# Kernel tuning notes

Hardware: AMD Instinct MI355X
Metric: run time of the kernel (lower is better)

The kernel has to match this reference:

```python
import jax, jax.numpy as jnp
import numpy as np

ALPHA = 4.0   # spikingjelly surrogate.Sigmoid default
TAU = 2.0
VTH = 1.0
EPS = 1e-5

@jax.custom_vjp
def spike(x):
    return (x >= 0.0).astype(x.dtype)

def _spike_fwd(x):
    return spike(x), x

def _spike_bwd(x, g):
    s = jax.nn.sigmoid(ALPHA * x)
    return (g * ALPHA * s * (1.0 - s),)

spike.defvjp(_spike_fwd, _spike_bwd)

def lif(x):
    # x: [T, B, N, C]; multi-step LIF, v_reset=0 hard reset, detach_reset=True
    def step(v, xt):
        v = v + (xt - v) / TAU          # charge
        s = spike(v - VTH)              # fire (surrogate grad)
        v = v * (1.0 - jax.lax.stop_gradient(s))  # hard reset, detached
        return v, s
    _, out = jax.lax.scan(step, jnp.zeros_like(x[0]), x)
    return out

def bn(x, gamma, beta):
    # BatchNorm1d in training mode: per-channel (last dim) over all other dims
    mu = x.mean(axis=(0, 1, 2), keepdims=True)
    var = x.var(axis=(0, 1, 2), keepdims=True)  # biased var, as torch BN uses for normalization
    return (x - mu) * jax.lax.rsqrt(var + EPS) * gamma + beta

def setup_inputs() -> dict:
    key = jax.random.key(0)
    ks = jax.random.split(key, 3)
    T, B, N, C, H = 4, 32, 1024, 256, 256
    x = jax.random.normal(ks[0], (T, B, N, C), dtype=jnp.float32)
    W1 = jax.random.normal(ks[1], (C, H), dtype=jnp.float32) * (1.0 / np.sqrt(C))
    W2 = jax.random.normal(ks[2], (H, C), dtype=jnp.float32) * (1.0 / np.sqrt(H))
    return {
        "x": x,
        "W1": W1, "b1": jnp.zeros((H,), jnp.float32),
        "gamma1": jnp.ones((H,), jnp.float32), "beta1": jnp.zeros((H,), jnp.float32),
        "W2": W2, "b2": jnp.zeros((C,), jnp.float32),
        "gamma2": jnp.ones((C,), jnp.float32), "beta2": jnp.zeros((C,), jnp.float32),
    }

def reference(x, W1, b1, gamma1, beta1, W2, b2, gamma2, beta2):
    # fc1: Linear -> BN (per-channel over T*B*N) -> multi-step LIF
    h = jnp.einsum('tbnc,ch->tbnh', x, W1) + b1
    h = lif(bn(h, gamma1, beta1))
    # fc2
    o = jnp.einsum('tbnh,ho->tbno', h, W2) + b2
    return lif(bn(o, gamma2, beta2))
```

## Files before the change

kernel.cpp:

```cpp
#include <hip/hip_runtime.h>


typedef __attribute__((ext_vector_type(8))) short bf16x8;
typedef __attribute__((ext_vector_type(8))) _Float16 f16x8;
typedef __attribute__((ext_vector_type(4))) _Float16 f16x4;
typedef __attribute__((ext_vector_type(4))) float f32x4;

__device__ __forceinline__ unsigned short f32_to_bf16_rne(float f) {
    unsigned int u = __builtin_bit_cast(unsigned int, f);
    u += 0x7FFFu + ((u >> 16) & 1u);
    return (unsigned short)(u >> 16);
}
__device__ __forceinline__ float bf16_to_f32(unsigned short h) {
    unsigned int u = ((unsigned int)h) << 16;
    return __builtin_bit_cast(float, u);
}
__device__ __forceinline__ int xcd_swz(int bid, int nwg) {
    int per = nwg >> 3;
    return (bid & 7) * per + (bid >> 3);
}

__global__ __launch_bounds__(256) void split_w1(const float* __restrict__ W1,
                                                _Float16* __restrict__ BhiT,
                                                _Float16* __restrict__ BloT) {
    int i = blockIdx.x * 256 + threadIdx.x;
    int k = i >> 8, n = i & 255;
    float w = W1[i];
    _Float16 hi = (_Float16)w;
    _Float16 lo = (_Float16)((w - (float)hi) * 4096.0f);
    BhiT[(size_t)n * 256 + k] = hi;
    BloT[(size_t)n * 256 + k] = lo;
}

__global__ __launch_bounds__(256) void split_w2(const float* __restrict__ W2,
                                                unsigned short* __restrict__ Bt) {
    int i = blockIdx.x * 256 + threadIdx.x;
    int k = i >> 8, n = i & 255;
    float w = W2[i];
    unsigned short hi = f32_to_bf16_rne(w);
    float r = w - bf16_to_f32(hi);
    unsigned short mid = f32_to_bf16_rne(r);
    float r2 = r - bf16_to_f32(mid);
    unsigned short lo = f32_to_bf16_rne(r2);
    Bt[(size_t)(0 * 256 + n) * 256 + k] = hi;
    Bt[(size_t)(1 * 256 + n) * 256 + k] = mid;
    Bt[(size_t)(2 * 256 + n) * 256 + k] = lo;
}

__global__ __launch_bounds__(256, 2) void gemm1_mfma(const float* __restrict__ A,
                                                     const _Float16* __restrict__ Bhi,
                                                     const _Float16* __restrict__ Blo,
                                                     const float* __restrict__ bias,
                                                     float* __restrict__ C,
                                                     double* __restrict__ partial) {
    __shared__ __align__(16) _Float16 Ahi[64 * 256];
    __shared__ __align__(16) _Float16 Alo[64 * 256];
    const int blk = xcd_swz(blockIdx.x, gridDim.x);
    const size_t m0 = (size_t)blk * 64;
    const int tid = threadIdx.x;
    const int lane = tid & 63;
    const int wc = tid >> 6;
    const int lrow = lane & 15, lchunk = lane >> 4;

    const _Float16* BhiB = Bhi + ((size_t)(64 * wc + lrow)) * 256 + lchunk * 8;
    const _Float16* BloB = Blo + ((size_t)(64 * wc + lrow)) * 256 + lchunk * 8;

    f16x8 bh[2][4], bl[2][4];
#define LOADB1(buf, kk)                                                   \
    _Pragma("unroll") for (int nf = 0; nf < 4; ++nf) {                    \
        bh[buf][nf] = *(const f16x8*)(BhiB + nf * 4096 + (kk) * 32);      \
        bl[buf][nf] = *(const f16x8*)(BloB + nf * 4096 + (kk) * 32);      \
    }

    LOADB1(0, 0)

    {
        const float* src = A + m0 * 256;
        float4 rr[16];
#pragma unroll
        for (int it = 0; it < 16; ++it)
            rr[it] = *(const float4*)(src + (size_t)(it * 256 + tid) * 4);
#pragma unroll
        for (int it = 0; it < 16; ++it) {
            unsigned i4 = (unsigned)(it * 256 + tid);
            float f[4] = {rr[it].x, rr[it].y, rr[it].z, rr[it].w};
            f16x4 hi4, lo4;
#pragma unroll
            for (int e = 0; e < 4; ++e) {
                _Float16 hh = (_Float16)f[e];
                hi4[e] = hh;
                lo4[e] = (_Float16)((f[e] - (float)hh) * 4096.0f);
            }
            unsigned off = i4 * 8u;
            unsigned swz = off ^ (((off >> 9) & 7u) << 4);
            *(f16x4*)((char*)Ahi + swz) = hi4;
            *(f16x4*)((char*)Alo + swz) = lo4;
        }
    }
    __syncthreads();

    f32x4 acc0[4][4] = {}, acc1[4][4] = {};

#pragma unroll
    for (int k0 = 0; k0 < 8; ++k0) {
        const int cur = k0 & 1;
        if (k0 < 7) { LOADB1(cur ^ 1, k0 + 1) }
        f16x8 ah[4], al[4];
#pragma unroll
        for (int mf = 0; mf < 4; ++mf) {
            unsigned r = (unsigned)(16 * mf + lrow);
            unsigned off = (r * 512u + (unsigned)(k0 * 64 + lchunk * 16)) ^ ((r & 7u) << 4);
            ah[mf] = *(const f16x8*)((const char*)Ahi + off);
            al[mf] = *(const f16x8*)((const char*)Alo + off);
        }
        __builtin_amdgcn_s_setprio(1);
#pragma unroll
        for (int nf = 0; nf < 4; ++nf)
#pragma unroll
            for (int mf = 0; mf < 4; ++mf)
                acc0[mf][nf] = __builtin_amdgcn_mfma_f32_16x16x32_f16(
                    ah[mf], bh[cur][nf], acc0[mf][nf], 0, 0, 0);
#pragma unroll
        for (int nf = 0; nf < 4; ++nf)
#pragma unroll
            for (int mf = 0; mf < 4; ++mf)
                acc1[mf][nf] = __builtin_amdgcn_mfma_f32_16x16x32_f16(
                    ah[mf], bl[cur][nf], acc1[mf][nf], 0, 0, 0);
#pragma unroll
        for (int nf = 0; nf < 4; ++nf)
#pragma unroll
            for (int mf = 0; mf < 4; ++mf)
                acc1[mf][nf] = __builtin_amdgcn_mfma_f32_16x16x32_f16(
                    al[mf], bh[cur][nf], acc1[mf][nf], 0, 0, 0);
        __builtin_amdgcn_s_setprio(0);
    }
#undef LOADB1

    const float UNSCALE = 1.0f / 4096.0f;
#pragma unroll
    for (int nf = 0; nf < 4; ++nf) {
        int col = 64 * wc + 16 * nf + lrow;
        float bvv = bias[col];
        double ss = 0.0, qq = 0.0;
#pragma unroll
        for (int mf = 0; mf < 4; ++mf) {
            size_t rowb = m0 + 16 * mf + 4 * lchunk;
#pragma unroll
            for (int e = 0; e < 4; ++e) {
                float hv = acc0[mf][nf][e] + acc1[mf][nf][e] * UNSCALE + bvv;
                C[(rowb + e) * 256 + col] = hv;
                ss += (double)hv;
                qq += (double)hv * (double)hv;
            }
        }
        ss += __shfl_xor(ss, 16);
        ss += __shfl_xor(ss, 32);
        qq += __shfl_xor(qq, 16);
        qq += __shfl_xor(qq, 32);
        if (lane < 16) {
            partial[(size_t)blk * 512 + col] = ss;
            partial[(size_t)blk * 512 + 256 + col] = qq;
        }
    }
}

__global__ __launch_bounds__(256, 2) void gemm2_fused(const float* __restrict__ h,
                                                      const float2* __restrict__ ss1,
                                                      const unsigned short* __restrict__ Bt,
                                                      const float* __restrict__ bias,
                                                      float* __restrict__ C,
                                                      double* __restrict__ partial,
                                                      int bnRows) {
    __shared__ __align__(16) unsigned short Asw[64 * 256];
    const int blk = xcd_swz(blockIdx.x, gridDim.x);
    const int bn0 = blk * 16;
    const int tid = threadIdx.x;
    const int lane = tid & 63;
    const int wc = tid >> 6;
    const int lrow = lane & 15, lchunk = lane >> 4;

    const unsigned short* Bbase =
        Bt + ((size_t)(64 * wc + lrow)) * 256 + lchunk * 8;

    bf16x8 bb[2][12];
#define LOADB(buf, kk)                                                        \
    _Pragma("unroll") for (int t_ = 0; t_ < 3; ++t_)                          \
    _Pragma("unroll") for (int nf = 0; nf < 4; ++nf)                          \
        bb[buf][t_ * 4 + nf] = *(const bf16x8*)(Bbase + (size_t)t_ * 65536 +  \
                                                nf * 4096 + (kk) * 32);

    LOADB(0, 0)

    {
        float4 rr[16];
#pragma unroll
        for (int it = 0; it < 4; ++it) {
            int slot = it * 256 + tid;
            int bn = slot >> 6;
            int colq = slot & 63;
            size_t rb = (size_t)(bn0 + bn) * 256 + colq * 4;
#pragma unroll
            for (int t4 = 0; t4 < 4; ++t4)
                rr[it * 4 + t4] = *(const float4*)(h + (size_t)t4 * bnRows * 256 + rb);
        }
#pragma unroll
        for (int it = 0; it < 4; ++it) {
            int slot = it * 256 + tid;
            int bn = slot >> 6;
            int colq = slot & 63;
            int c0 = colq * 4;
            float2 p0 = ss1[c0], p1 = ss1[c0 + 1], p2 = ss1[c0 + 2], p3 = ss1[c0 + 3];
            float4 v = make_float4(0.f, 0.f, 0.f, 0.f);
#pragma unroll
            for (int t4 = 0; t4 < 4; ++t4) {
                float4 hv = rr[it * 4 + t4];
                float x0 = hv.x * p0.x + p0.y;
                float x1 = hv.y * p1.x + p1.y;
                float x2 = hv.z * p2.x + p2.y;
                float x3 = hv.w * p3.x + p3.y;
                v.x = (v.x + x0) * 0.5f;
                v.y = (v.y + x1) * 0.5f;
                v.z = (v.z + x2) * 0.5f;
                v.w = (v.w + x3) * 0.5f;
                ushort4 sp;
                sp.x = (v.x >= 1.0f) ? 0x3F80 : 0;
                sp.y = (v.y >= 1.0f) ? 0x3F80 : 0;
                sp.z = (v.z >= 1.0f) ? 0x3F80 : 0;
                sp.w = (v.w >= 1.0f) ? 0x3F80 : 0;
                v.x = (v.x >= 1.0f) ? 0.0f : v.x;
                v.y = (v.y >= 1.0f) ? 0.0f : v.y;
                v.z = (v.z >= 1.0f) ? 0.0f : v.z;
                v.w = (v.w >= 1.0f) ? 0.0f : v.w;
                unsigned row = (unsigned)(t4 * 16 + bn);
                unsigned off = (row * 512u + (unsigned)colq * 8u) ^ ((row & 7u) << 4);
                *(ushort4*)((char*)Asw + off) = sp;
            }
        }
    }
    __syncthreads();

    f32x4 acc[4][4] = {};

#pragma unroll
    for (int k0 = 0; k0 < 8; ++k0) {
        const int cur = k0 & 1;
        if (k0 < 7) { LOADB(cur ^ 1, k0 + 1) }
        bf16x8 af[4];
#pragma unroll
        for (int mf = 0; mf < 4; ++mf) {
            unsigned r = (unsigned)(16 * mf + lrow);
            unsigned off = (r * 512u + (unsigned)(k0 * 64 + lchunk * 16)) ^ ((r & 7u) << 4);
            af[mf] = *(const bf16x8*)((const char*)Asw + off);
        }
        __builtin_amdgcn_s_setprio(1);
#pragma unroll
        for (int t_ = 0; t_ < 3; ++t_)
#pragma unroll
            for (int nf = 0; nf < 4; ++nf)
#pragma unroll
                for (int mf = 0; mf < 4; ++mf)
                    acc[mf][nf] = __builtin_amdgcn_mfma_f32_16x16x32_bf16(
                        af[mf], bb[cur][t_ * 4 + nf], acc[mf][nf], 0, 0, 0);
        __builtin_amdgcn_s_setprio(0);
    }
#undef LOADB

#pragma unroll
    for (int nf = 0; nf < 4; ++nf) {
        int col = 64 * wc + 16 * nf + lrow;
        float bvv = bias[col];
        double ss = 0.0, qq = 0.0;
#pragma unroll
        for (int mf = 0; mf < 4; ++mf) {
            int Lbase = 16 * mf + 4 * lchunk;
#pragma unroll
            for (int e = 0; e < 4; ++e) {
                int L = Lbase + e;
                size_t G = (size_t)(L >> 4) * bnRows + bn0 + (L & 15);
                float hv = acc[mf][nf][e] + bvv;
                C[G * 256 + col] = hv;
                ss += (double)hv;
                qq += (double)hv * (double)hv;
            }
        }
        ss += __shfl_xor(ss, 16);
        ss += __shfl_xor(ss, 32);
        qq += __shfl_xor(qq, 16);
        qq += __shfl_xor(qq, 32);
        if (lane < 16) {
            partial[(size_t)blk * 512 + col] = ss;
            partial[(size_t)blk * 512 + 256 + col] = qq;
        }
    }
}

__global__ __launch_bounds__(256) void finalize_stats(const double* __restrict__ partial,
                                                      const float* __restrict__ gamma,
                                                      const float* __restrict__ beta,
                                                      float2* __restrict__ ss,
                                                      int nblocks, double invM) {
    const int c = blockIdx.x;
    const int t = threadIdx.x;
    __shared__ double sh[256];
    __shared__ double sh2[256];
    double s = 0.0, s2 = 0.0;
    for (int b = t; b < nblocks; b += 256) {
        s += partial[(size_t)b * 512 + c];
        s2 += partial[(size_t)b * 512 + 256 + c];
    }
    sh[t] = s;
    sh2[t] = s2;
    __syncthreads();
#pragma unroll
    for (int off = 128; off > 0; off >>= 1) {
        if (t < off) {
            sh[t] += sh[t + off];
            sh2[t] += sh2[t + off];
        }
        __syncthreads();
    }
    if (t == 0) {
        double mu = sh[0] * invM;
        double var = sh2[0] * invM - mu * mu;
        double rstd = 1.0 / sqrt(var + 1e-5);
        double sc = (double)gamma[c] * rstd;
        ss[c] = make_float2((float)sc, (float)((double)beta[c] - mu * sc));
    }
}

__global__ __launch_bounds__(256) void bnlif_f32(const float* __restrict__ h,
                                                 const float2* __restrict__ ss,
                                                 float* __restrict__ out,
                                                 int slab4) {
    int t4 = blockIdx.x * 256 + threadIdx.x;
    if (t4 >= slab4) return;
    size_t idx = (size_t)t4 * 4;
    int c0 = (int)(idx & 255);
    float2 p0 = ss[c0], p1 = ss[c0 + 1], p2 = ss[c0 + 2], p3 = ss[c0 + 3];
    size_t slab = (size_t)slab4 * 4;
    float4 v = make_float4(0.f, 0.f, 0.f, 0.f);
#pragma unroll
    for (int t = 0; t < 4; ++t) {
        float4 hv = *(const float4*)(h + (size_t)t * slab + idx);
        float x0 = hv.x * p0.x + p0.y;
        float x1 = hv.y * p1.x + p1.y;
        float x2 = hv.z * p2.x + p2.y;
        float x3 = hv.w * p3.x + p3.y;
        v.x = (v.x + x0) * 0.5f;
        v.y = (v.y + x1) * 0.5f;
        v.z = (v.z + x2) * 0.5f;
        v.w = (v.w + x3) * 0.5f;
        float4 sp;
        sp.x = (v.x >= 1.0f) ? 1.0f : 0.0f;
        sp.y = (v.y >= 1.0f) ? 1.0f : 0.0f;
        sp.z = (v.z >= 1.0f) ? 1.0f : 0.0f;
        sp.w = (v.w >= 1.0f) ? 1.0f : 0.0f;
        v.x = (v.x >= 1.0f) ? 0.0f : v.x;
        v.y = (v.y >= 1.0f) ? 0.0f : v.y;
        v.z = (v.z >= 1.0f) ? 0.0f : v.z;
        v.w = (v.w >= 1.0f) ? 0.0f : v.w;
        *(float4*)(out + (size_t)t * slab + idx) = sp;
    }
}

extern "C" void kernel_launch(void* const* d_in, const int* in_sizes, int n_in,
                              void* d_out, int out_size, void* d_ws, size_t ws_size,
                              hipStream_t stream) {
    const float* x  = (const float*)d_in[0];
    const float* W1 = (const float*)d_in[1];
    const float* b1 = (const float*)d_in[2];
    const float* g1 = (const float*)d_in[3];
    const float* be1 = (const float*)d_in[4];
    const float* W2 = (const float*)d_in[5];
    const float* b2 = (const float*)d_in[6];
    const float* g2 = (const float*)d_in[7];
    const float* be2 = (const float*)d_in[8];
    float* out = (float*)d_out;

    const int M = in_sizes[0] / 256;
    const int bnRows = M / 4;
    const size_t hBytes = (size_t)M * 256 * 4;

    char* ws = (char*)d_ws;
    float* h = (float*)ws;
    double* partial = (double*)(ws + hBytes);
    unsigned short* W2catT = (unsigned short*)(ws + hBytes + (size_t)2048 * 512 * 8);
    float2* ss1 = (float2*)((char*)W2catT + 3 * 256 * 256 * 2);
    float2* ss2 = ss1 + 256;
    _Float16* W1hiT = (_Float16*)(ss2 + 256);
    _Float16* W1loT = W1hiT + 256 * 256;

    const int slab4 = M * 16;
    const double invM = 1.0 / (double)M;
    const int NB1 = M / 64;
    const int NB2 = bnRows / 16;

    dim3 blk(256);

    split_w1<<<dim3(256), blk, 0, stream>>>(W1, W1hiT, W1loT);
    split_w2<<<dim3(256), blk, 0, stream>>>(W2, W2catT);

    gemm1_mfma<<<dim3(NB1), blk, 0, stream>>>(x, W1hiT, W1loT, b1, h, partial);
    finalize_stats<<<dim3(256), blk, 0, stream>>>(partial, g1, be1, ss1, NB1, invM);

    gemm2_fused<<<dim3(NB2), blk, 0, stream>>>(h, ss1, W2catT, b2, h, partial, bnRows);
    finalize_stats<<<dim3(256), blk, 0, stream>>>(partial, g2, be2, ss2, NB2, invM);
    bnlif_f32<<<dim3(slab4 / 256), blk, 0, stream>>>(h, ss2, out, slab4);
}
```

Before: 301.0 us.

## Use 512-thread blocks with 8 waves splitting N in both GEMM kernels

Both GEMM kernels now launch 512 threads (8 waves), and each wave computes a 64x32 output slice instead of 64x64. This halves per-wave accumulators and B-fragment registers. The B-operand register double-buffering is dropped in favour of loading B at the start of each k-step. The aim is more resident waves per CU to hide memory latency, with fewer registers per thread. The cost is more exposed global-load latency for B inside the k loop and more LDS reads of A, since each wave re-reads the full A tile for fewer columns.

```diff
diff --git a/kernel.cpp b/kernel.cpp
--- a/kernel.cpp
+++ b/kernel.cpp
@@ -47,7 +47,7 @@
     Bt[(size_t)(2 * 256 + n) * 256 + k] = lo;
 }
 
-__global__ __launch_bounds__(256, 2) void gemm1_mfma(const float* __restrict__ A,
+__global__ __launch_bounds__(512, 4) void gemm1_mfma(const float* __restrict__ A,
                                                      const _Float16* __restrict__ Bhi,
                                                      const _Float16* __restrict__ Blo,
                                                      const float* __restrict__ bias,
@@ -59,30 +59,21 @@
     const size_t m0 = (size_t)blk * 64;
     const int tid = threadIdx.x;
     const int lane = tid & 63;
-    const int wc = tid >> 6;
+    const int wave = tid >> 6;
     const int lrow = lane & 15, lchunk = lane >> 4;
 
-    const _Float16* BhiB = Bhi + ((size_t)(64 * wc + lrow)) * 256 + lchunk * 8;
-    const _Float16* BloB = Blo + ((size_t)(64 * wc + lrow)) * 256 + lchunk * 8;
-
-    f16x8 bh[2][4], bl[2][4];
-#define LOADB1(buf, kk)                                                   \
-    _Pragma("unroll") for (int nf = 0; nf < 4; ++nf) {                    \
-        bh[buf][nf] = *(const f16x8*)(BhiB + nf * 4096 + (kk) * 32);      \
-        bl[buf][nf] = *(const f16x8*)(BloB + nf * 4096 + (kk) * 32);      \
-    }
-
-    LOADB1(0, 0)
+    const _Float16* BhiB = Bhi + ((size_t)(32 * wave + lrow)) * 256 + lchunk * 8;
+    const _Float16* BloB = Blo + ((size_t)(32 * wave + lrow)) * 256 + lchunk * 8;
 
     {
         const float* src = A + m0 * 256;
-        float4 rr[16];
-#pragma unroll
-        for (int it = 0; it < 16; ++it)
-            rr[it] = *(const float4*)(src + (size_t)(it * 256 + tid) * 4);
-#pragma unroll
-        for (int it = 0; it < 16; ++it) {
-            unsigned i4 = (unsigned)(it * 256 + tid);
+        float4 rr[8];
+#pragma unroll
+        for (int it = 0; it < 8; ++it)
+            rr[it] = *(const float4*)(src + (size_t)(it * 512 + tid) * 4);
+#pragma unroll
+        for (int it = 0; it < 8; ++it) {
+            unsigned i4 = (unsigned)(it * 512 + tid);
             float f[4] = {rr[it].x, rr[it].y, rr[it].z, rr[it].w};
             f16x4 hi4, lo4;
 #pragma unroll
@@ -99,47 +90,47 @@
     }
     __syncthreads();
 
-    f32x4 acc0[4][4] = {}, acc1[4][4] = {};
+    f32x4 acc0[4][2] = {}, acc1[4][2] = {};
 
 #pragma unroll
     for (int k0 = 0; k0 < 8; ++k0) {
-        const int cur = k0 & 1;
-        if (k0 < 7) { LOADB1(cur ^ 1, k0 + 1) }
-        f16x8 ah[4], al[4];
-#pragma unroll
-        for (int mf = 0; mf < 4; ++mf) {
-            unsigned r = (unsigned)(16 * mf + lrow);
-            unsigned off = (r * 512u + (unsigned)(k0 * 64 + lchunk * 16)) ^ ((r & 7u) << 4);
-            ah[mf] = *(const f16x8*)((const char*)Ahi + off);
-            al[mf] = *(const f16x8*)((const char*)Alo + off);
-        }
-        __builtin_amdgcn_s_setprio(1);
-#pragma unroll
-        for (int nf = 0; nf < 4; ++nf)
-#pragma unroll
-            for (int mf = 0; mf < 4; ++mf)
-                acc0[mf][nf] = __builtin_amdgcn_mfma_f32_16x16x32_f16(
-                    ah[mf], bh[cur][nf], acc0[mf][nf], 0, 0, 0);
-#pragma unroll
-        for (int nf = 0; nf < 4; ++nf)
-#pragma unroll
-            for (int mf = 0; mf < 4; ++mf)
-                acc1[mf][nf] = __builtin_amdgcn_mfma_f32_16x16x32_f16(
-                    ah[mf], bl[cur][nf], acc1[mf][nf], 0, 0, 0);
-#pragma unroll
-        for (int nf = 0; nf < 4; ++nf)
-#pragma unroll
-            for (int mf = 0; mf < 4; ++mf)
-                acc1[mf][nf] = __builtin_amdgcn_mfma_f32_16x16x32_f16(
-                    al[mf], bh[cur][nf], acc1[mf][nf], 0, 0, 0);
-        __builtin_amdgcn_s_setprio(0);
-    }
-#undef LOADB1
+        f16x8 bh[2], bl[2];
+#pragma unroll
+        for (int nf = 0; nf < 2; ++nf) {
+            bh[nf] = *(const f16x8*)(BhiB + nf * 4096 + k0 * 32);
+            bl[nf] = *(const f16x8*)(BloB + nf * 4096 + k0 * 32);
+        }
+#pragma unroll
+        for (int half = 0; half < 2; ++half) {
+            f16x8 ah[2], al[2];
+#pragma unroll
+            for (int m = 0; m < 2; ++m) {
+                unsigned r = (unsigned)(32 * half + 16 * m + lrow);
+                unsigned off = (r * 512u + (unsigned)(k0 * 64 + lchunk * 16)) ^ ((r & 7u) << 4);
+                ah[m] = *(const f16x8*)((const char*)Ahi + off);
+                al[m] = *(const f16x8*)((const char*)Alo + off);
+            }
+            __builtin_amdgcn_s_setprio(1);
+#pragma unroll
+            for (int nf = 0; nf < 2; ++nf)
+#pragma unroll
+                for (int m = 0; m < 2; ++m) {
+                    const int mf = half * 2 + m;
+                    acc0[mf][nf] = __builtin_amdgcn_mfma_f32_16x16x32_f16(
+                        ah[m], bh[nf], acc0[mf][nf], 0, 0, 0);
+                    acc1[mf][nf] = __builtin_amdgcn_mfma_f32_16x16x32_f16(
+                        ah[m], bl[nf], acc1[mf][nf], 0, 0, 0);
+                    acc1[mf][nf] = __builtin_amdgcn_mfma_f32_16x16x32_f16(
+                        al[m], bh[nf], acc1[mf][nf], 0, 0, 0);
+                }
+            __builtin_amdgcn_s_setprio(0);
+        }
+    }
 
     const float UNSCALE = 1.0f / 4096.0f;
 #pragma unroll
-    for (int nf = 0; nf < 4; ++nf) {
-        int col = 64 * wc + 16 * nf + lrow;
+    for (int nf = 0; nf < 2; ++nf) {
+        int col = 32 * wave + 16 * nf + lrow;
         float bvv = bias[col];
         double ss = 0.0, qq = 0.0;
 #pragma unroll
@@ -164,7 +155,7 @@
     }
 }
 
-__global__ __launch_bounds__(256, 2) void gemm2_fused(const float* __restrict__ h,
+__global__ __launch_bounds__(512, 4) void gemm2_fused(const float* __restrict__ h,
                                                       const float2* __restrict__ ss1,
                                                       const unsigned short* __restrict__ Bt,
                                                       const float* __restrict__ bias,
@@ -176,26 +167,17 @@
     const int bn0 = blk * 16;
     const int tid = threadIdx.x;
     const int lane = tid & 63;
-    const int wc = tid >> 6;
+    const int wave = tid >> 6;
     const int lrow = lane & 15, lchunk = lane >> 4;
 
     const unsigned short* Bbase =
-        Bt + ((size_t)(64 * wc + lrow)) * 256 + lchunk * 8;
-
-    bf16x8 bb[2][12];
-#define LOADB(buf, kk)                                                        \
-    _Pragma("unroll") for (int t_ = 0; t_ < 3; ++t_)                          \
-    _Pragma("unroll") for (int nf = 0; nf < 4; ++nf)                          \
-        bb[buf][t_ * 4 + nf] = *(const bf16x8*)(Bbase + (size_t)t_ * 65536 +  \
-                                                nf * 4096 + (kk) * 32);
-
-    LOADB(0, 0)
+        Bt + ((size_t)(32 * wave + lrow)) * 256 + lchunk * 8;
 
     {
-        float4 rr[16];
-#pragma unroll
-        for (int it = 0; it < 4; ++it) {
-            int slot = it * 256 + tid;
+        float4 rr[8];
+#pragma unroll
+        for (int it = 0; it < 2; ++it) {
+            int slot = it * 512 + tid;
             int bn = slot >> 6;
             int colq = slot & 63;
             size_t rb = (size_t)(bn0 + bn) * 256 + colq * 4;
@@ -204,8 +186,8 @@
                 rr[it * 4 + t4] = *(const float4*)(h + (size_t)t4 * bnRows * 256 + rb);
         }
 #pragma unroll
-        for (int it = 0; it < 4; ++it) {
-            int slot = it * 256 + tid;
+        for (int it = 0; it < 2; ++it) {
+            int slot = it * 512 + tid;
             int bn = slot >> 6;
             int colq = slot & 63;
             int c0 = colq * 4;
@@ -239,35 +221,44 @@
     }
     __syncthreads();
 
-    f32x4 acc[4][4] = {};
+    f32x4 acc[4][2] = {};
 
 #pragma unroll
     for (int k0 = 0; k0 < 8; ++k0) {
-        const int cur = k0 & 1;
-        if (k0 < 7) { LOADB(cur ^ 1, k0 + 1) }
-        bf16x8 af[4];
-#pragma unroll
-        for (int mf = 0; mf < 4; ++mf) {
-            unsigned r = (unsigned)(16 * mf + lrow);
-            unsigned off = (r * 512u + (unsigned)(k0 * 64 + lchunk * 16)) ^ ((r & 7u) << 4);
-            af[mf] = *(const bf16x8*)((const char*)Asw + off);
-        }
-        __builtin_amdgcn_s_setprio(1);
+        bf16x8 bb[6];
 #pragma unroll
         for (int t_ = 0; t_ < 3; ++t_)
 #pragma unroll
-            for (int nf = 0; nf < 4; ++nf)
-#pragma unroll
-                for (int mf = 0; mf < 4; ++mf)
-                    acc[mf][nf] = __builtin_amdgcn_mfma_f32_16x16x32_bf16(
-                        af[mf], bb[cur][t_ * 4 + nf], acc[mf][nf], 0, 0, 0);
-        __builtin_amdgcn_s_setprio(0);
-    }
-#undef LOADB
-
-#pragma unroll
-    for (int nf = 0; nf < 4; ++nf) {
-        int col = 64 * wc + 16 * nf + lrow;
+            for (int nf = 0; nf < 2; ++nf)
+                bb[t_ * 2 + nf] = *(const bf16x8*)(Bbase + (size_t)t_ * 65536 +
+                                                   nf * 4096 + k0 * 32);
+#pragma unroll
+        for (int half = 0; half < 2; ++half) {
+            bf16x8 af[2];
+#pragma unroll
+            for (int m = 0; m < 2; ++m) {
+                unsigned r = (unsigned)(32 * half + 16 * m + lrow);
+                unsigned off = (r * 512u + (unsigned)(k0 * 64 + lchunk * 16)) ^ ((r & 7u) << 4);
+                af[m] = *(const bf16x8*)((const char*)Asw + off);
+            }
+            __builtin_amdgcn_s_setprio(1);
+#pragma unroll
+            for (int t_ = 0; t_ < 3; ++t_)
+#pragma unroll
+                for (int nf = 0; nf < 2; ++nf)
+#pragma unroll
+                    for (int m = 0; m < 2; ++m) {
+                        const int mf = half * 2 + m;
+                        acc[mf][nf] = __builtin_amdgcn_mfma_f32_16x16x32_bf16(
+                            af[m], bb[t_ * 2 + nf], acc[mf][nf], 0, 0, 0);
+                    }
+            __builtin_amdgcn_s_setprio(0);
+        }
+    }
+
+#pragma unroll
+    for (int nf = 0; nf < 2; ++nf) {
+        int col = 32 * wave + 16 * nf + lrow;
         float bvv = bias[col];
         double ss = 0.0, qq = 0.0;
 #pragma unroll
@@ -400,10 +391,10 @@
     split_w1<<<dim3(256), blk, 0, stream>>>(W1, W1hiT, W1loT);
     split_w2<<<dim3(256), blk, 0, stream>>>(W2, W2catT);
 
-    gemm1_mfma<<<dim3(NB1), blk, 0, stream>>>(x, W1hiT, W1loT, b1, h, partial);
+    gemm1_mfma<<<dim3(NB1), dim3(512), 0, stream>>>(x, W1hiT, W1loT, b1, h, partial);
     finalize_stats<<<dim3(256), blk, 0, stream>>>(partial, g1, be1, ss1, NB1, invM);
 
-    gemm2_fused<<<dim3(NB2), blk, 0, stream>>>(h, ss1, W2catT, b2, h, partial, bnRows);
+    gemm2_fused<<<dim3(NB2), dim3(512), 0, stream>>>(h, ss1, W2catT, b2, h, partial, bnRows);
     finalize_stats<<<dim3(256), blk, 0, stream>>>(partial, g2, be2, ss2, NB2, invM);
     bnlif_f32<<<dim3(slab4 / 256), blk, 0, stream>>>(h, ss2, out, slab4);
 }
```

Result: faster. 290.7 us (median of 2 runs) (-3.4%).
